# Kernel optimization log

Hardware: AMD Instinct MI355X
Metric: run time of the kernel (lower is better)

## Reference

```python
import jax, jax.numpy as jnp
import numpy as np
import math

NUM_HEADS = 16
HEAD_DIM = 128
ROPE_BASE = 10000.0


def setup_inputs() -> dict:
    key = jax.random.key(0)
    ks = jax.random.split(key, 6)
    B, S, H = 2, 2048, 2048
    hidden_states = jax.random.normal(ks[0], (B, S, H), dtype=jnp.float32) * 0.02
    # causal additive mask, shape (B, 1, S, S)
    neg = jnp.finfo(jnp.float32).min
    causal = jnp.where(jnp.tril(jnp.ones((S, S), dtype=bool)), 0.0, neg).astype(jnp.float32)
    attention_mask = jnp.broadcast_to(causal[None, None], (B, 1, S, S))
    position_ids = jnp.broadcast_to(jnp.arange(S, dtype=jnp.int64)[None], (B, S))
    scale = 1.0 / math.sqrt(H)
    Wq = jax.random.normal(ks[1], (H, H), dtype=jnp.float32) * scale
    Wk = jax.random.normal(ks[2], (H, H), dtype=jnp.float32) * scale
    Wv = jax.random.normal(ks[3], (H, H), dtype=jnp.float32) * scale
    Wo = jax.random.normal(ks[4], (H, H), dtype=jnp.float32) * scale
    return {"hidden_states": hidden_states, "attention_mask": attention_mask,
            "position_ids": position_ids, "Wq": Wq, "Wk": Wk, "Wv": Wv, "Wo": Wo}


def _rotate_half(x):
    x1, x2 = jnp.split(x, 2, axis=-1)
    return jnp.concatenate((-x2, x1), axis=-1)


def reference(hidden_states, attention_mask, position_ids, Wq, Wk, Wv, Wo):
    B, S, H = hidden_states.shape
    nh, hd = NUM_HEADS, HEAD_DIM

    def shape_heads(x):  # (B,S,H) -> (B,nh,S,hd)
        return x.reshape(B, S, nh, hd).transpose(0, 2, 1, 3)

    q = shape_heads(hidden_states @ Wq.T)
    k = shape_heads(hidden_states @ Wk.T)
    v = shape_heads(hidden_states @ Wv.T)

    kv_seq_len = S  # no past_key_value
    # rotary table: (kv_seq_len, hd)
    inv_freq = 1.0 / (ROPE_BASE ** (jnp.arange(0, hd, 2, dtype=jnp.float32) / hd))
    t = jnp.arange(kv_seq_len, dtype=jnp.float32)
    freqs = jnp.einsum('i,j->ij', t, inv_freq)
    emb = jnp.concatenate((freqs, freqs), axis=-1)
    # gather-based RoPE == table lookup at position_ids: (B,S,hd) -> (B,1,S,hd)
    cos = jnp.cos(emb)[position_ids][:, None]
    sin = jnp.sin(emb)[position_ids][:, None]

    q = q * cos + _rotate_half(q) * sin
    k = k * cos + _rotate_half(k) * sin

    scores = jnp.einsum('bhqd,bhkd->bhqk', q, k) / math.sqrt(hd)
    scores = scores + attention_mask
    scores = jnp.maximum(scores, jnp.finfo(scores.dtype).min)
    probs = jax.nn.softmax(scores.astype(jnp.float32), axis=-1).astype(q.dtype)
    attn = jnp.einsum('bhqk,bhkd->bhqd', probs, v)  # (B,nh,S,hd)
    attn = attn.transpose(0, 2, 1, 3).reshape(B, S, H)
    return attn @ Wo.T
```

## Files before the change

kernel.cpp:

```cpp
#include <hip/hip_runtime.h>
#include <hip/hip_bf16.h>
#include <cstdint>

#define SQ    2048
#define HDIM  2048
#define NH    16
#define HD    128
#define BATCH 2
#define MTOK  (BATCH*SQ)

typedef unsigned short u16;
typedef unsigned int   u32;
typedef __bf16 bf16x8 __attribute__((ext_vector_type(8)));
typedef float  f32x4  __attribute__((ext_vector_type(4)));
typedef float  f32x16 __attribute__((ext_vector_type(16)));
typedef unsigned short u16x4 __attribute__((ext_vector_type(4)));
typedef unsigned int   u32x4 __attribute__((ext_vector_type(4)));

__device__ __forceinline__ u16 f2b(float f) {
  union { float f; unsigned u; } v; v.f = f;
  return (u16)((v.u + 0x7fffu + ((v.u >> 16) & 1u)) >> 16);
}
__device__ __forceinline__ float b2f(u16 b) {
  union { unsigned u; float f; } v; v.u = ((unsigned)b) << 16;
  return v.f;
}

#define GLD_LDS16(gp, lp) __builtin_amdgcn_global_load_lds( \
    (const __attribute__((address_space(1))) uint32_t*)(gp), \
    (__attribute__((address_space(3))) uint32_t*)(lp), 16, 0, 0)

__device__ __forceinline__ f32x16 zero16() {
  f32x16 v;
#pragma unroll
  for (int i = 0; i < 16; ++i) v[i] = 0.f;
  return v;
}

__global__ __launch_bounds__(256) void conv_bf16(const float* __restrict__ in,
                                                 u16* __restrict__ out, int n4) {
  int i = blockIdx.x * 256 + threadIdx.x;
  if (i >= n4) return;
  float4 v = ((const float4*)in)[i];
  u16x4 o;
  o.x = f2b(v.x); o.y = f2b(v.y); o.z = f2b(v.z); o.w = f2b(v.w);
  *(u16x4*)(out + (size_t)i * 4) = o;
}

__global__ __launch_bounds__(256) void conv_w4(const float* __restrict__ w0,
                                               const float* __restrict__ w1,
                                               const float* __restrict__ w2,
                                               const float* __restrict__ w3,
                                               u16* o0, u16* o1, u16* o2, u16* o3) {
  int i = blockIdx.x * 256 + threadIdx.x;
  int sel = blockIdx.y;
  const float* in = sel == 0 ? w0 : sel == 1 ? w1 : sel == 2 ? w2 : w3;
  u16* out = sel == 0 ? o0 : sel == 1 ? o1 : sel == 2 ? o2 : o3;
  float4 v = ((const float4*)in)[i];
  u16x4 o;
  o.x = f2b(v.x); o.y = f2b(v.y); o.z = f2b(v.z); o.w = f2b(v.w);
  *(u16x4*)(out + (size_t)i * 4) = o;
}

__global__ __launch_bounds__(256) void addk(const float* __restrict__ a,
                                            const float* __restrict__ b,
                                            float* __restrict__ o) {
  int i = blockIdx.x * 256 + threadIdx.x;
  float4 x = ((const float4*)a)[i], y = ((const float4*)b)[i];
  float4 r; r.x = x.x + y.x; r.y = x.y + y.y; r.z = x.z + y.z; r.w = x.w + y.w;
  ((float4*)o)[i] = r;
}

__global__ void rope_table_k(float* __restrict__ ct, float* __restrict__ st) {
  int s = blockIdx.x, j = threadIdx.x;
  float invf = expf(-(float)j * (9.210340371976184f / 64.0f));
  float ang = (float)s * invf;
  ct[s * 64 + j] = cosf(ang);
  st[s * 64 + j] = sinf(ang);
}

__global__ __launch_bounds__(256) void rope_apply2(u16* __restrict__ Xq,
                                                   u16* __restrict__ Xk,
                                                   const float* __restrict__ ct,
                                                   const float* __restrict__ st) {
  u16* X = blockIdx.y ? Xk : Xq;
  int idx = blockIdx.x * 256 + threadIdx.x;
  int j = idx & 63;
  int row = idx >> 6;
  int s = row & (SQ - 1);
  size_t base = (size_t)row * HD;
  float x1 = b2f(X[base + j]), x2 = b2f(X[base + j + 64]);
  float c = ct[s * 64 + j], sn = st[s * 64 + j];
  X[base + j]      = f2b(x1 * c - x2 * sn);
  X[base + j + 64] = f2b(x2 * c + x1 * sn);
}

template<int OUT>
__global__ __launch_bounds__(512, 1)
void gemm8m(const u16* __restrict__ A, const u16* __restrict__ W0,
            const u16* __restrict__ W1, const u16* __restrict__ W2,
            u16* __restrict__ oQ, u16* __restrict__ oK, u16* __restrict__ oV,
            float* __restrict__ oF, float* __restrict__ oF2, int nt) {
  __shared__ u16 Ah[2][2][128 * 64];
  __shared__ u16 Bh[2][2][128 * 64];
  const int tid = threadIdx.x, lane = tid & 63, w = tid >> 6;
  const int wm = w >> 2, wn = w & 3;
  const int gx = gridDim.x;
  const int lin = blockIdx.y * gx + blockIdx.x;
  const int cpx = (gx * gridDim.y) >> 3;
  const int swz = (lin & 7) * cpx + (lin >> 3);
  const int bx = swz % gx, by = swz / gx;
  const int m0 = by * 256;
  const int n0g = bx * 256;
  const int kbase = (OUT == 1) ? (int)blockIdx.z * 1024 : 0;
  int sel; const u16* Bw; int nloc;
  if (OUT == 0) {
    sel = n0g >> 11;
    Bw = (sel == 0) ? W0 : (sel == 1) ? W1 : W2;
    nloc = n0g & 2047;
  } else {
    sel = 0; Bw = W0; nloc = n0g;
  }
  float* dstF = (OUT == 1) ? (blockIdx.z ? oF2 : oF) : oF;

  u32 aoff[2][2], boff[2][2];
#pragma unroll
  for (int h = 0; h < 2; ++h) {
#pragma unroll
    for (int l = 0; l < 2; ++l) {
      int c = l * 512 + tid, ra = c >> 3, sl = c & 7;
      int r = ((ra >> 6) << 7) + h * 64 + (ra & 63);
      aoff[h][l] = (u32)((m0 + r) * HDIM + kbase + ((sl ^ (ra & 7)) * 8));
      int col = nloc + ((ra >> 5) * 64) + h * 32 + (ra & 31);
      boff[h][l] = (u32)(col * HDIM + kbase + ((sl ^ (ra & 7)) * 8));
    }
  }
  auto stageA = [&](int buf, int h, int k0) {
#pragma unroll
    for (int l = 0; l < 2; ++l)
      GLD_LDS16(A + (size_t)aoff[h][l] + k0, &Ah[buf][h][(l * 512 + tid) * 8]);
  };
  auto stageB = [&](int buf, int h, int k0) {
#pragma unroll
    for (int l = 0; l < 2; ++l)
      GLD_LDS16(Bw + (size_t)boff[h][l] + k0, &Bh[buf][h][(l * 512 + tid) * 8]);
  };

  f32x4 acc[8][4];
#pragma unroll
  for (int i = 0; i < 8; ++i)
#pragma unroll
    for (int j = 0; j < 4; ++j) acc[i][j] = (f32x4){0.f, 0.f, 0.f, 0.f};

  const int l15 = lane & 15, hi4 = lane >> 4;
  const int swr = (l15 & 7) << 4;

  bf16x8 afv0[4][2], afv1[4][2];
  bf16x8 bfv0[2][2], bfv1[2][2];

  auto readA = [&](bf16x8 (&dst)[4][2], const char* Ab) {
#pragma unroll
    for (int j = 0; j < 4; ++j)
#pragma unroll
      for (int kk = 0; kk < 2; ++kk)
        dst[j][kk] = *(const bf16x8*)(Ab + (wm * 64 + j * 16 + l15) * 128 +
                                      ((kk * 64 + hi4 * 16) ^ swr));
  };
  auto readB = [&](bf16x8 (&dst)[2][2], const char* Bb) {
#pragma unroll
    for (int j2 = 0; j2 < 2; ++j2)
#pragma unroll
      for (int kk = 0; kk < 2; ++kk)
        dst[j2][kk] = *(const bf16x8*)(Bb + (wn * 32 + j2 * 16 + l15) * 128 +
                                       ((kk * 64 + hi4 * 16) ^ swr));
  };
  auto mfq = [&](bf16x8 (&af)[4][2], bf16x8 (&bf)[2][2], int mh, int nh) {
#pragma unroll
    for (int kk = 0; kk < 2; ++kk)
#pragma unroll
      for (int j = 0; j < 4; ++j)
#pragma unroll
        for (int j2 = 0; j2 < 2; ++j2)
          acc[mh * 4 + j][nh * 2 + j2] = __builtin_amdgcn_mfma_f32_16x16x32_bf16(
              af[j][kk], bf[j2][kk], acc[mh * 4 + j][nh * 2 + j2], 0, 0, 0);
  };

  stageA(0, 0, 0); stageB(0, 0, 0); stageA(0, 1, 0); stageB(0, 1, 0);
  asm volatile("s_waitcnt vmcnt(4)" ::: "memory");
  __builtin_amdgcn_s_barrier();

  for (int t = 0; t < nt; ++t) {
    const int cur = t & 1, nb = cur ^ 1;
    const bool st = (t + 1 < nt);
    const int kn = (t + 1) * 64;
    const char* Ab0 = (const char*)&Ah[cur][0][0];
    const char* Ab1 = (const char*)&Ah[cur][1][0];
    const char* Bb0 = (const char*)&Bh[cur][0][0];
    const char* Bb1 = (const char*)&Bh[cur][1][0];

    readA(afv0, Ab0); readB(bfv0, Bb0);
    if (st) {
      stageA(nb, 0, kn); stageB(nb, 0, kn);
      asm volatile("s_waitcnt vmcnt(6)" ::: "memory");
    } else {
      asm volatile("s_waitcnt vmcnt(2)" ::: "memory");
    }
    __builtin_amdgcn_s_barrier();
    asm volatile("s_waitcnt lgkmcnt(0)" ::: "memory");
    __builtin_amdgcn_sched_barrier(0);
    __builtin_amdgcn_s_setprio(1); mfq(afv0, bfv0, 0, 0); __builtin_amdgcn_s_setprio(0);

    readA(afv1, Ab1);
    if (st) {
      stageA(nb, 1, kn);
      asm volatile("s_waitcnt vmcnt(6)" ::: "memory");
    } else {
      asm volatile("s_waitcnt vmcnt(0)" ::: "memory");
    }
    __builtin_amdgcn_s_barrier();
    asm volatile("s_waitcnt lgkmcnt(0)" ::: "memory");
    __builtin_amdgcn_sched_barrier(0);
    __builtin_amdgcn_s_setprio(1); mfq(afv1, bfv0, 1, 0); __builtin_amdgcn_s_setprio(0);

    readB(bfv1, Bb1);
    if (st) stageB(nb, 1, kn);
    __builtin_amdgcn_s_barrier();
    asm volatile("s_waitcnt lgkmcnt(0)" ::: "memory");
    __builtin_amdgcn_sched_barrier(0);
    __builtin_amdgcn_s_setprio(1); mfq(afv0, bfv1, 0, 1); __builtin_amdgcn_s_setprio(0);

    if (st) asm volatile("s_waitcnt vmcnt(4)" ::: "memory");
    __builtin_amdgcn_s_barrier();
    __builtin_amdgcn_s_setprio(1); mfq(afv1, bfv1, 1, 1); __builtin_amdgcn_s_setprio(0);
  }

  const int cl = l15, rg = hi4 * 4;
#pragma unroll
  for (int mi = 0; mi < 8; ++mi) {
#pragma unroll
    for (int ni = 0; ni < 4; ++ni) {
      const int mb = m0 + wm * 128 + mi * 16 + rg;
      const int n = nloc + wn * 64 + ni * 16 + cl;
      if (OUT == 1) {
#pragma unroll
        for (int r = 0; r < 4; ++r)
          dstF[(size_t)(mb + r) * HDIM + n] = acc[mi][ni][r];
      } else {
        const int h = n >> 7, d = n & 127;
        if (sel == 2) {
          const int b = mb >> 11, s = mb & (SQ - 1);
          u16x4 pk;
          pk.x = f2b(acc[mi][ni][0]); pk.y = f2b(acc[mi][ni][1]);
          pk.z = f2b(acc[mi][ni][2]); pk.w = f2b(acc[mi][ni][3]);
          *(u16x4*)&oV[((size_t)(b * NH + h) * HD + d) * SQ + s] = pk;
        } else {
          u16* O = sel ? oK : oQ;
#pragma unroll
          for (int r = 0; r < 4; ++r) {
            const int m = mb + r, b = m >> 11, s = m & (SQ - 1);
            O[((size_t)(b * NH + h) * SQ + s) * HD + d] = f2b(acc[mi][ni][r]);
          }
        }
      }
    }
  }
}

__device__ __forceinline__ void stage_kv(u16* ksb, u16* vsb,
                                         const u16* __restrict__ Kg,
                                         const u16* __restrict__ Vg,
                                         int kv0, int w, int lane) {
#pragma unroll
  for (int i = 0; i < 4; ++i) {
    int chunk = (w * 4 + i) * 64 + lane;
    int row = chunk >> 4, c16 = chunk & 15;
    int csrc = c16 ^ (row & 7);
    GLD_LDS16(Kg + (size_t)(kv0 + row) * HD + csrc * 8, ksb + (w * 4 + i) * 512);
  }
#pragma unroll
  for (int i = 0; i < 4; ++i) {
    int chunk = (w * 4 + i) * 64 + lane;
    int d = chunk >> 3, c8 = chunk & 7;
    int csrc = c8 ^ (d & 7);
    GLD_LDS16(Vg + (size_t)d * SQ + kv0 + csrc * 8, vsb + (w * 4 + i) * 512);
  }
}

#define MKPA(dst, P, off) { \
  u32 u0_, u1_, u2_, u3_; \
  asm("v_cvt_pk_bf16_f32 %0, %1, %2" : "=v"(u0_) : "v"(P[off + 0]), "v"(P[off + 1])); \
  asm("v_cvt_pk_bf16_f32 %0, %1, %2" : "=v"(u1_) : "v"(P[off + 2]), "v"(P[off + 3])); \
  asm("v_cvt_pk_bf16_f32 %0, %1, %2" : "=v"(u2_) : "v"(P[off + 4]), "v"(P[off + 5])); \
  asm("v_cvt_pk_bf16_f32 %0, %1, %2" : "=v"(u3_) : "v"(P[off + 6]), "v"(P[off + 7])); \
  u32 x0_ = (u32)__shfl_xor((int)u0_, 32, 64); \
  u32 x1_ = (u32)__shfl_xor((int)u1_, 32, 64); \
  u32 x2_ = (u32)__shfl_xor((int)u2_, 32, 64); \
  u32 x3_ = (u32)__shfl_xor((int)u3_, 32, 64); \
  u32x4 w_; \
  w_.x = hi ? x2_ : u0_; \
  w_.y = hi ? x3_ : u1_; \
  w_.z = hi ? u2_ : x0_; \
  w_.w = hi ? u3_ : x1_; \
  dst = __builtin_bit_cast(bf16x8, w_); \
}

#define PVD(oD, dblk) { \
  const int dr_ = (dblk) * 32 + l31; \
  const int sw_ = (dr_ & 7) << 4; \
  bf16x8 v0_ = *(const bf16x8*)(Vb + ((dr_ * 128 +  0 + hi * 16) ^ sw_)); \
  oD = __builtin_amdgcn_mfma_f32_32x32x16_bf16(pa[0], v0_, oD, 0, 0, 0); \
  bf16x8 v1_ = *(const bf16x8*)(Vb + ((dr_ * 128 + 32 + hi * 16) ^ sw_)); \
  oD = __builtin_amdgcn_mfma_f32_32x32x16_bf16(pa[1], v1_, oD, 0, 0, 0); \
  bf16x8 v2_ = *(const bf16x8*)(Vb + ((dr_ * 128 + 64 + hi * 16) ^ sw_)); \
  oD = __builtin_amdgcn_mfma_f32_32x32x16_bf16(pa[2], v2_, oD, 0, 0, 0); \
  bf16x8 v3_ = *(const bf16x8*)(Vb + ((dr_ * 128 + 96 + hi * 16) ^ sw_)); \
  oD = __builtin_amdgcn_mfma_f32_32x32x16_bf16(pa[3], v3_, oD, 0, 0, 0); \
}

__global__ __launch_bounds__(256, 2)
void flash_fwd2(const u16* __restrict__ Q, const u16* __restrict__ K,
                const u16* __restrict__ Vt, u16* __restrict__ Out) {
  __shared__ u16 Ks[2][64 * 128];
  __shared__ u16 Vs[2][128 * 64];
  const int tid = threadIdx.x, lane = tid & 63, w = tid >> 6;
  const int hi = lane >> 5, l31 = lane & 31;
  const int qt = 15 - (int)(blockIdx.x >> 5);
  const int bh = blockIdx.x & 31;
  const int q0 = qt * 128;
  const u16* Qg = Q + (size_t)bh * SQ * HD;
  const u16* Kg = K + (size_t)bh * SQ * HD;
  const u16* Vg = Vt + (size_t)bh * HD * SQ;
  const int qw = q0 + w * 32;
  const int qg = qw + l31;

  bf16x8 qf[8];
#pragma unroll
  for (int st = 0; st < 8; ++st)
    qf[st] = *(const bf16x8*)&Qg[(size_t)qg * HD + st * 16 + hi * 8];

  f32x16 o0 = zero16(), o1 = zero16(), o2 = zero16(), o3 = zero16();
  float lsum = 0.f;
  const float sL2E = 0.1275174446f;
  const int ktl = 2 * qt + 1;
  int cur = 0;

  stage_kv(Ks[0], Vs[0], Kg, Vg, 0, w, lane);

  for (int kt = 0; kt <= ktl; ++kt) {
    if (kt < ktl) {
      stage_kv(Ks[cur ^ 1], Vs[cur ^ 1], Kg, Vg, (kt + 1) * 64, w, lane);
      asm volatile("s_waitcnt vmcnt(8)" ::: "memory");
    } else {
      asm volatile("s_waitcnt vmcnt(0)" ::: "memory");
    }
    __builtin_amdgcn_s_barrier();

    const int kv0 = kt * 64;
    if (kv0 <= qw + 31) {
      const char* Kb = (const char*)Ks[cur];
      const char* Vb = (const char*)Vs[cur];
      f32x16 c0 = zero16(), c1 = zero16();
      const int kr0 = l31, kr1 = 32 + l31;
      const int sw0 = (kr0 & 7) << 4;
#pragma unroll
      for (int st = 0; st < 8; ++st) {
        bf16x8 k0 = *(const bf16x8*)(Kb + ((kr0 * 256 + st * 32 + hi * 16) ^ sw0));
        c0 = __builtin_amdgcn_mfma_f32_32x32x16_bf16(k0, qf[st], c0, 0, 0, 0);
        bf16x8 k1 = *(const bf16x8*)(Kb + ((kr1 * 256 + st * 32 + hi * 16) ^ sw0));
        c1 = __builtin_amdgcn_mfma_f32_32x32x16_bf16(k1, qf[st], c1, 0, 0, 0);
      }
      const bool needmask = (kv0 + 63 > qw);
      const int lim0 = qg - kv0, lim1 = lim0 - 32;
      if (needmask) {
#pragma unroll
        for (int r = 0; r < 16; ++r) {
          const int cr = (r & 3) + 8 * (r >> 2) + 4 * hi;
          float p0 = exp2f(c0[r] * sL2E);
          c0[r] = (cr <= lim0) ? p0 : 0.f;
          float p1 = exp2f(c1[r] * sL2E);
          c1[r] = (cr <= lim1) ? p1 : 0.f;
          lsum += c0[r] + c1[r];
        }
      } else {
#pragma unroll
        for (int r = 0; r < 16; ++r) {
          c0[r] = exp2f(c0[r] * sL2E);
          c1[r] = exp2f(c1[r] * sL2E);
          lsum += c0[r] + c1[r];
        }
      }
      bf16x8 pa[4];
      MKPA(pa[0], c0, 0); MKPA(pa[1], c0, 8);
      MKPA(pa[2], c1, 0); MKPA(pa[3], c1, 8);
      PVD(o0, 0) PVD(o1, 1) PVD(o2, 2) PVD(o3, 3)
    }
    __builtin_amdgcn_s_barrier();
    cur ^= 1;
  }

  float ltot = lsum + __shfl_xor(lsum, 32, 64);
  float invl = 1.f / ltot;
  const int b = bh >> 4, h = bh & 15;
#pragma unroll
  for (int g = 0; g < 4; ++g) {
#pragma unroll
    for (int j = 0; j < 4; ++j) {
      const int r = g * 4 + j;
      const int cr = g * 8 + 4 * hi + j;
      float inv = __shfl(invl, cr, 64);
      const int s = q0 + w * 32 + cr;
      size_t rb = ((size_t)(b * SQ + s)) * HDIM + h * HD;
      Out[rb +  0 + l31] = f2b(o0[r] * inv);
      Out[rb + 32 + l31] = f2b(o1[r] * inv);
      Out[rb + 64 + l31] = f2b(o2[r] * inv);
      Out[rb + 96 + l31] = f2b(o3[r] * inv);
    }
  }
}

extern "C" void kernel_launch(void* const* d_in, const int* in_sizes, int n_in,
                              void* d_out, int out_size, void* d_ws, size_t ws_size,
                              hipStream_t stream) {
  const float* hs = (const float*)d_in[0];
  const float* Wq = (const float*)d_in[3];
  const float* Wk = (const float*)d_in[4];
  const float* Wv = (const float*)d_in[5];
  const float* Wo = (const float*)d_in[6];

  char* ws = (char*)d_ws;
  u16* XB  = (u16*)(ws);
  u16* WQB = (u16*)(ws + (size_t)(16 << 20));
  u16* WKB = (u16*)(ws + (size_t)(24 << 20));
  u16* WVB = (u16*)(ws + (size_t)(32 << 20));
  u16* WOB = (u16*)(ws + (size_t)(40 << 20));
  u16* QR  = (u16*)(ws + (size_t)(48 << 20));
  u16* KR  = (u16*)(ws + (size_t)(64 << 20));
  u16* VT  = (u16*)(ws + (size_t)(80 << 20));
  u16* ATT = (u16*)(ws + (size_t)(96 << 20));
  float* CT = (float*)(ws + (size_t)(112 << 20));
  float* ST = (float*)(ws + (size_t)(112 << 20) + (1 << 19));
  float* P0 = (float*)(ws);
  float* P1 = (float*)(ws + (size_t)(48 << 20));

  conv_bf16<<<8192, 256, 0, stream>>>(hs, XB, 2097152);
  conv_w4<<<dim3(4096, 4), 256, 0, stream>>>(Wq, Wk, Wv, Wo, WQB, WKB, WVB, WOB);
  rope_table_k<<<SQ, 64, 0, stream>>>(CT, ST);

  gemm8m<0><<<dim3(24, 16), 512, 0, stream>>>(XB, WQB, WKB, WVB,
                                              QR, KR, VT, nullptr, nullptr, 32);

  rope_apply2<<<dim3(16384, 2), 256, 0, stream>>>(QR, KR, CT, ST);

  flash_fwd2<<<512, 256, 0, stream>>>(QR, KR, VT, ATT);

  gemm8m<1><<<dim3(8, 16, 2), 512, 0, stream>>>(ATT, WOB, nullptr, nullptr,
                                                nullptr, nullptr, nullptr,
                                                P0, P1, 16);
  addk<<<8192, 256, 0, stream>>>(P0, P1, (float*)d_out);
}
```

Baseline: 276.3 us.

## Split QKV GEMM into QK and V launches, enlarge flash attention tiles

The fused QKV GEMM is split in two: a 256-row-tile kernel for Q/K and a 128-row-tile kernel for V, each launched on a 1D grid of 256 blocks, which is meant to balance waves across the CUs. Flash attention moves to 512-thread blocks covering 256 queries each, so every staged K/V tile is reused across more queries. V now uses a single buffer that is loaded after the PV step, while K stays double-buffered, with extra barriers and waitcnts between the two. The K swizzle changes from 8 to 16 rows. The occupancy target is raised to 4 blocks of 512 threads, which may strain registers, and the single V buffer may expose load latency.

```diff
diff --git a/kernel.cpp b/kernel.cpp
--- a/kernel.cpp
+++ b/kernel.cpp
@@ -95,49 +95,55 @@
   X[base + j + 64] = f2b(x2 * c + x1 * sn);
 }
 
-template<int OUT>
+template<int BM, int MODE>
 __global__ __launch_bounds__(512, 1)
-void gemm8m(const u16* __restrict__ A, const u16* __restrict__ W0,
-            const u16* __restrict__ W1, const u16* __restrict__ W2,
-            u16* __restrict__ oQ, u16* __restrict__ oK, u16* __restrict__ oV,
-            float* __restrict__ oF, float* __restrict__ oF2, int nt) {
-  __shared__ u16 Ah[2][2][128 * 64];
+void gemmT(const u16* __restrict__ A, const u16* __restrict__ W0,
+           const u16* __restrict__ W1,
+           u16* __restrict__ oQ, u16* __restrict__ oK, u16* __restrict__ oV,
+           float* __restrict__ oF, float* __restrict__ oF2,
+           int nt, int gx) {
+  constexpr int MH  = (BM == 256) ? 4 : 2;
+  constexpr int ALH = (BM == 256) ? 2 : 1;
+  constexpr int WUS = (BM == 256) ? 6 : 5;
+  __shared__ u16 Ah[2][2][(BM / 2) * 64];
   __shared__ u16 Bh[2][2][128 * 64];
   const int tid = threadIdx.x, lane = tid & 63, w = tid >> 6;
   const int wm = w >> 2, wn = w & 3;
-  const int gx = gridDim.x;
-  const int lin = blockIdx.y * gx + blockIdx.x;
-  const int cpx = (gx * gridDim.y) >> 3;
+  int lin, kbase, nblk;
+  if (MODE == 1) {
+    lin = blockIdx.y * gx + blockIdx.x; kbase = blockIdx.z * 1024;
+    nblk = gx * gridDim.y;
+  } else {
+    lin = blockIdx.x; kbase = 0; nblk = gridDim.x;
+  }
+  const int cpx = nblk >> 3;
   const int swz = (lin & 7) * cpx + (lin >> 3);
   const int bx = swz % gx, by = swz / gx;
-  const int m0 = by * 256;
-  const int n0g = bx * 256;
-  const int kbase = (OUT == 1) ? (int)blockIdx.z * 1024 : 0;
+  const int m0 = by * BM, n0g = bx * 256;
   int sel; const u16* Bw; int nloc;
-  if (OUT == 0) {
-    sel = n0g >> 11;
-    Bw = (sel == 0) ? W0 : (sel == 1) ? W1 : W2;
-    nloc = n0g & 2047;
-  } else {
-    sel = 0; Bw = W0; nloc = n0g;
-  }
-  float* dstF = (OUT == 1) ? (blockIdx.z ? oF2 : oF) : oF;
-
-  u32 aoff[2][2], boff[2][2];
+  if (MODE == 0) { sel = n0g >> 11; Bw = sel ? W1 : W0; nloc = n0g & 2047; }
+  else { sel = (MODE == 2) ? 2 : 0; Bw = W0; nloc = n0g; }
+  float* dstF = (MODE == 1) ? (blockIdx.z ? oF2 : oF) : oF;
+
+  u32 aoff[2][ALH], boff[2][2];
 #pragma unroll
   for (int h = 0; h < 2; ++h) {
 #pragma unroll
+    for (int l = 0; l < ALH; ++l) {
+      int c = l * 512 + tid, ra = c >> 3, sl = c & 7;
+      int r = ((ra >> WUS) << (WUS + 1)) + h * (BM / 4) + (ra & (BM / 4 - 1));
+      aoff[h][l] = (u32)((m0 + r) * HDIM + kbase + ((sl ^ (ra & 7)) * 8));
+    }
+#pragma unroll
     for (int l = 0; l < 2; ++l) {
-      int c = l * 512 + tid, ra = c >> 3, sl = c & 7;
-      int r = ((ra >> 6) << 7) + h * 64 + (ra & 63);
-      aoff[h][l] = (u32)((m0 + r) * HDIM + kbase + ((sl ^ (ra & 7)) * 8));
-      int col = nloc + ((ra >> 5) * 64) + h * 32 + (ra & 31);
-      boff[h][l] = (u32)(col * HDIM + kbase + ((sl ^ (ra & 7)) * 8));
+      int c = l * 512 + tid, cb = c >> 3, sl = c & 7;
+      int col = nloc + ((cb >> 5) * 64) + h * 32 + (cb & 31);
+      boff[h][l] = (u32)(col * HDIM + kbase + ((sl ^ (cb & 7)) * 8));
     }
   }
   auto stageA = [&](int buf, int h, int k0) {
 #pragma unroll
-    for (int l = 0; l < 2; ++l)
+    for (int l = 0; l < ALH; ++l)
       GLD_LDS16(A + (size_t)aoff[h][l] + k0, &Ah[buf][h][(l * 512 + tid) * 8]);
   };
   auto stageB = [&](int buf, int h, int k0) {
@@ -146,24 +152,24 @@
       GLD_LDS16(Bw + (size_t)boff[h][l] + k0, &Bh[buf][h][(l * 512 + tid) * 8]);
   };
 
-  f32x4 acc[8][4];
-#pragma unroll
-  for (int i = 0; i < 8; ++i)
+  f32x4 acc[2 * MH][4];
+#pragma unroll
+  for (int i = 0; i < 2 * MH; ++i)
 #pragma unroll
     for (int j = 0; j < 4; ++j) acc[i][j] = (f32x4){0.f, 0.f, 0.f, 0.f};
 
   const int l15 = lane & 15, hi4 = lane >> 4;
   const int swr = (l15 & 7) << 4;
 
-  bf16x8 afv0[4][2], afv1[4][2];
+  bf16x8 afv0[MH][2], afv1[MH][2];
   bf16x8 bfv0[2][2], bfv1[2][2];
 
-  auto readA = [&](bf16x8 (&dst)[4][2], const char* Ab) {
-#pragma unroll
-    for (int j = 0; j < 4; ++j)
+  auto readA = [&](bf16x8 (&dst)[MH][2], const char* Ab) {
+#pragma unroll
+    for (int j = 0; j < MH; ++j)
 #pragma unroll
       for (int kk = 0; kk < 2; ++kk)
-        dst[j][kk] = *(const bf16x8*)(Ab + (wm * 64 + j * 16 + l15) * 128 +
+        dst[j][kk] = *(const bf16x8*)(Ab + (wm * (BM / 4) + j * 16 + l15) * 128 +
                                       ((kk * 64 + hi4 * 16) ^ swr));
   };
   auto readB = [&](bf16x8 (&dst)[2][2], const char* Bb) {
@@ -174,19 +180,20 @@
         dst[j2][kk] = *(const bf16x8*)(Bb + (wn * 32 + j2 * 16 + l15) * 128 +
                                        ((kk * 64 + hi4 * 16) ^ swr));
   };
-  auto mfq = [&](bf16x8 (&af)[4][2], bf16x8 (&bf)[2][2], int mh, int nh) {
+  auto mfq = [&](bf16x8 (&af)[MH][2], bf16x8 (&bf)[2][2], int mh, int nh) {
 #pragma unroll
     for (int kk = 0; kk < 2; ++kk)
 #pragma unroll
-      for (int j = 0; j < 4; ++j)
+      for (int j = 0; j < MH; ++j)
 #pragma unroll
         for (int j2 = 0; j2 < 2; ++j2)
-          acc[mh * 4 + j][nh * 2 + j2] = __builtin_amdgcn_mfma_f32_16x16x32_bf16(
-              af[j][kk], bf[j2][kk], acc[mh * 4 + j][nh * 2 + j2], 0, 0, 0);
+          acc[mh * MH + j][nh * 2 + j2] = __builtin_amdgcn_mfma_f32_16x16x32_bf16(
+              af[j][kk], bf[j2][kk], acc[mh * MH + j][nh * 2 + j2], 0, 0, 0);
   };
 
   stageA(0, 0, 0); stageB(0, 0, 0); stageA(0, 1, 0); stageB(0, 1, 0);
-  asm volatile("s_waitcnt vmcnt(4)" ::: "memory");
+  if constexpr (BM == 256) asm volatile("s_waitcnt vmcnt(4)" ::: "memory");
+  else                     asm volatile("s_waitcnt vmcnt(3)" ::: "memory");
   __builtin_amdgcn_s_barrier();
 
   for (int t = 0; t < nt; ++t) {
@@ -201,7 +208,8 @@
     readA(afv0, Ab0); readB(bfv0, Bb0);
     if (st) {
       stageA(nb, 0, kn); stageB(nb, 0, kn);
-      asm volatile("s_waitcnt vmcnt(6)" ::: "memory");
+      if constexpr (BM == 256) asm volatile("s_waitcnt vmcnt(6)" ::: "memory");
+      else                     asm volatile("s_waitcnt vmcnt(5)" ::: "memory");
     } else {
       asm volatile("s_waitcnt vmcnt(2)" ::: "memory");
     }
@@ -213,7 +221,8 @@
     readA(afv1, Ab1);
     if (st) {
       stageA(nb, 1, kn);
-      asm volatile("s_waitcnt vmcnt(6)" ::: "memory");
+      if constexpr (BM == 256) asm volatile("s_waitcnt vmcnt(6)" ::: "memory");
+      else                     asm volatile("s_waitcnt vmcnt(4)" ::: "memory");
     } else {
       asm volatile("s_waitcnt vmcnt(0)" ::: "memory");
     }
@@ -229,19 +238,22 @@
     __builtin_amdgcn_sched_barrier(0);
     __builtin_amdgcn_s_setprio(1); mfq(afv0, bfv1, 0, 1); __builtin_amdgcn_s_setprio(0);
 
-    if (st) asm volatile("s_waitcnt vmcnt(4)" ::: "memory");
+    if (st) {
+      if constexpr (BM == 256) asm volatile("s_waitcnt vmcnt(4)" ::: "memory");
+      else                     asm volatile("s_waitcnt vmcnt(3)" ::: "memory");
+    }
     __builtin_amdgcn_s_barrier();
     __builtin_amdgcn_s_setprio(1); mfq(afv1, bfv1, 1, 1); __builtin_amdgcn_s_setprio(0);
   }
 
   const int cl = l15, rg = hi4 * 4;
 #pragma unroll
-  for (int mi = 0; mi < 8; ++mi) {
+  for (int mi = 0; mi < 2 * MH; ++mi) {
 #pragma unroll
     for (int ni = 0; ni < 4; ++ni) {
-      const int mb = m0 + wm * 128 + mi * 16 + rg;
+      const int mb = m0 + wm * (BM / 2) + mi * 16 + rg;
       const int n = nloc + wn * 64 + ni * 16 + cl;
-      if (OUT == 1) {
+      if (MODE == 1) {
 #pragma unroll
         for (int r = 0; r < 4; ++r)
           dstF[(size_t)(mb + r) * HDIM + n] = acc[mi][ni][r];
@@ -266,23 +278,24 @@
   }
 }
 
-__device__ __forceinline__ void stage_kv(u16* ksb, u16* vsb,
-                                         const u16* __restrict__ Kg,
-                                         const u16* __restrict__ Vg,
+__device__ __forceinline__ void stage_k8(u16* ksb, const u16* __restrict__ Kg,
                                          int kv0, int w, int lane) {
 #pragma unroll
-  for (int i = 0; i < 4; ++i) {
-    int chunk = (w * 4 + i) * 64 + lane;
+  for (int i = 0; i < 2; ++i) {
+    int chunk = (w * 2 + i) * 64 + lane;
     int row = chunk >> 4, c16 = chunk & 15;
-    int csrc = c16 ^ (row & 7);
-    GLD_LDS16(Kg + (size_t)(kv0 + row) * HD + csrc * 8, ksb + (w * 4 + i) * 512);
-  }
-#pragma unroll
-  for (int i = 0; i < 4; ++i) {
-    int chunk = (w * 4 + i) * 64 + lane;
+    int csrc = c16 ^ (row & 15);
+    GLD_LDS16(Kg + (size_t)(kv0 + row) * HD + csrc * 8, ksb + (w * 2 + i) * 512);
+  }
+}
+__device__ __forceinline__ void stage_v8(u16* vsb, const u16* __restrict__ Vg,
+                                         int kv0, int w, int lane) {
+#pragma unroll
+  for (int i = 0; i < 2; ++i) {
+    int chunk = (w * 2 + i) * 64 + lane;
     int d = chunk >> 3, c8 = chunk & 7;
     int csrc = c8 ^ (d & 7);
-    GLD_LDS16(Vg + (size_t)d * SQ + kv0 + csrc * 8, vsb + (w * 4 + i) * 512);
+    GLD_LDS16(Vg + (size_t)d * SQ + kv0 + csrc * 8, vsb + (w * 2 + i) * 512);
   }
 }
 
@@ -317,16 +330,16 @@
   oD = __builtin_amdgcn_mfma_f32_32x32x16_bf16(pa[3], v3_, oD, 0, 0, 0); \
 }
 
-__global__ __launch_bounds__(256, 2)
-void flash_fwd2(const u16* __restrict__ Q, const u16* __restrict__ K,
+__global__ __launch_bounds__(512, 4)
+void flash_fwd3(const u16* __restrict__ Q, const u16* __restrict__ K,
                 const u16* __restrict__ Vt, u16* __restrict__ Out) {
   __shared__ u16 Ks[2][64 * 128];
-  __shared__ u16 Vs[2][128 * 64];
+  __shared__ u16 Vs[128 * 64];
   const int tid = threadIdx.x, lane = tid & 63, w = tid >> 6;
   const int hi = lane >> 5, l31 = lane & 31;
-  const int qt = 15 - (int)(blockIdx.x >> 5);
+  const int qt = 7 - (int)(blockIdx.x >> 5);
   const int bh = blockIdx.x & 31;
-  const int q0 = qt * 128;
+  const int q0 = qt * 256;
   const u16* Qg = Q + (size_t)bh * SQ * HD;
   const u16* Kg = K + (size_t)bh * SQ * HD;
   const u16* Vg = Vt + (size_t)bh * HD * SQ;
@@ -341,27 +354,31 @@
   f32x16 o0 = zero16(), o1 = zero16(), o2 = zero16(), o3 = zero16();
   float lsum = 0.f;
   const float sL2E = 0.1275174446f;
-  const int ktl = 2 * qt + 1;
+  const int ktl = 4 * qt + 3;
   int cur = 0;
 
-  stage_kv(Ks[0], Vs[0], Kg, Vg, 0, w, lane);
+  stage_k8(Ks[0], Kg, 0, w, lane);
+  stage_v8(Vs, Vg, 0, w, lane);
+  asm volatile("s_waitcnt vmcnt(0)" ::: "memory");
+  __builtin_amdgcn_s_barrier();
 
   for (int kt = 0; kt <= ktl; ++kt) {
     if (kt < ktl) {
-      stage_kv(Ks[cur ^ 1], Vs[cur ^ 1], Kg, Vg, (kt + 1) * 64, w, lane);
-      asm volatile("s_waitcnt vmcnt(8)" ::: "memory");
+      stage_k8(Ks[cur ^ 1], Kg, (kt + 1) * 64, w, lane);
+      asm volatile("s_waitcnt vmcnt(4)" ::: "memory");
     } else {
-      asm volatile("s_waitcnt vmcnt(0)" ::: "memory");
+      asm volatile("s_waitcnt vmcnt(2)" ::: "memory");
     }
     __builtin_amdgcn_s_barrier();
 
     const int kv0 = kt * 64;
-    if (kv0 <= qw + 31) {
+    const bool act = (kv0 <= qw + 31);
+    bf16x8 pa[4];
+    if (act) {
       const char* Kb = (const char*)Ks[cur];
-      const char* Vb = (const char*)Vs[cur];
       f32x16 c0 = zero16(), c1 = zero16();
       const int kr0 = l31, kr1 = 32 + l31;
-      const int sw0 = (kr0 & 7) << 4;
+      const int sw0 = (l31 & 15) << 4;
 #pragma unroll
       for (int st = 0; st < 8; ++st) {
         bf16x8 k0 = *(const bf16x8*)(Kb + ((kr0 * 256 + st * 32 + hi * 16) ^ sw0));
@@ -389,12 +406,18 @@
           lsum += c0[r] + c1[r];
         }
       }
-      bf16x8 pa[4];
       MKPA(pa[0], c0, 0); MKPA(pa[1], c0, 8);
       MKPA(pa[2], c1, 0); MKPA(pa[3], c1, 8);
+    }
+    if (kt < ktl) asm volatile("s_waitcnt vmcnt(2)" ::: "memory");
+    else          asm volatile("s_waitcnt vmcnt(0)" ::: "memory");
+    __builtin_amdgcn_s_barrier();
+    if (act) {
+      const char* Vb = (const char*)Vs;
       PVD(o0, 0) PVD(o1, 1) PVD(o2, 2) PVD(o3, 3)
     }
     __builtin_amdgcn_s_barrier();
+    if (kt < ktl) stage_v8(Vs, Vg, (kt + 1) * 64, w, lane);
     cur ^= 1;
   }
 
@@ -446,15 +469,17 @@
   conv_w4<<<dim3(4096, 4), 256, 0, stream>>>(Wq, Wk, Wv, Wo, WQB, WKB, WVB, WOB);
   rope_table_k<<<SQ, 64, 0, stream>>>(CT, ST);
 
-  gemm8m<0><<<dim3(24, 16), 512, 0, stream>>>(XB, WQB, WKB, WVB,
-                                              QR, KR, VT, nullptr, nullptr, 32);
+  gemmT<256, 0><<<256, 512, 0, stream>>>(XB, WQB, WKB, QR, KR, nullptr,
+                                         nullptr, nullptr, 32, 16);
+  gemmT<128, 2><<<256, 512, 0, stream>>>(XB, WVB, nullptr, nullptr, nullptr, VT,
+                                         nullptr, nullptr, 32, 8);
 
   rope_apply2<<<dim3(16384, 2), 256, 0, stream>>>(QR, KR, CT, ST);
 
-  flash_fwd2<<<512, 256, 0, stream>>>(QR, KR, VT, ATT);
-
-  gemm8m<1><<<dim3(8, 16, 2), 512, 0, stream>>>(ATT, WOB, nullptr, nullptr,
-                                                nullptr, nullptr, nullptr,
-                                                P0, P1, 16);
+  flash_fwd3<<<256, 512, 0, stream>>>(QR, KR, VT, ATT);
+
+  gemmT<256, 1><<<dim3(8, 16, 2), 512, 0, stream>>>(ATT, WOB, nullptr,
+                                                    nullptr, nullptr, nullptr,
+                                                    P0, P1, 16, 8);
   addk<<<8192, 256, 0, stream>>>(P0, P1, (float*)d_out);
 }
```

After: 608.4 us. 120% more time.
